# Kernel tuning notes

Measured on AMD Instinct MI355X. Metric: run time of the kernel, lower is better.

## Reference

```python
import jax, jax.numpy as jnp
import numpy as np

B, L, D = 4096, 200, 64
N_ITEMS, N_USERS, N_RATINGS = 100000, 100000, 5


def setup_inputs() -> dict:
    key = jax.random.key(0)
    ks = jax.random.split(key, 10)
    nodes = jax.random.randint(ks[0], (B,), 0, N_USERS)
    history_uv = jax.random.randint(ks[1], (B, L), 0, N_ITEMS)
    history_r = jax.random.randint(ks[2], (B, L), 0, N_RATINGS)
    s = 1.0 / np.sqrt(D)
    v2e = jax.random.normal(ks[3], (N_ITEMS, D), dtype=jnp.float32)
    r2e = jax.random.normal(ks[4], (N_RATINGS, D), dtype=jnp.float32)
    # torch Linear: weight is [out, in]
    w1_W = jax.random.uniform(ks[5], (D, 2 * D), dtype=jnp.float32, minval=-s, maxval=s)
    w1_b = jax.random.uniform(ks[6], (D,), dtype=jnp.float32, minval=-s, maxval=s)
    w2_W = jax.random.uniform(ks[7], (D, D), dtype=jnp.float32, minval=-s, maxval=s)
    w2_b = jax.random.uniform(ks[8], (D,), dtype=jnp.float32, minval=-s, maxval=s)
    return {
        "v2e": v2e, "r2e": r2e,
        "w1_W": w1_W, "w1_b": w1_b, "w2_W": w2_W, "w2_b": w2_b,
        "nodes": nodes, "history_uv": history_uv, "history_r": history_r,
    }


def reference(v2e, r2e, w1_W, w1_b, w2_W, w2_b, nodes, history_uv, history_r):
    # Gather item and rating embeddings for every (node, history slot): [B, L, D]
    e_uv = v2e[history_uv]
    e_r = r2e[history_r]
    # concat -> [B, L, 2D], two-layer MLP with ReLU
    x = jnp.concatenate([e_uv, e_r], axis=-1)
    h = jax.nn.relu(jnp.einsum("bli,oi->blo", x, w1_W) + w1_b)
    o = jax.nn.relu(jnp.einsum("bli,oi->blo", h, w2_W) + w2_b)
    # uv=True branch: plain mean over the history dimension (nodes/u2e unused)
    return jnp.mean(o, axis=1)  # [B, D]
```

## Files before the change

kernel.cpp:

```cpp
#include <hip/hip_runtime.h>

#define NITEMS 100000
#define NRATE  5
#define BB     4096
#define LL     200
#define DD     64
#define NTILES 6250
#define NWAVES 2048

typedef short short8  __attribute__((ext_vector_type(8)));
typedef float f32x4   __attribute__((ext_vector_type(4)));
typedef float f32x2   __attribute__((ext_vector_type(2)));
typedef int   i32x4   __attribute__((ext_vector_type(4)));
typedef int   i32x2   __attribute__((ext_vector_type(2)));

static __device__ __forceinline__ short f2bf(float f) {
  return (short)((__builtin_bit_cast(unsigned, f) + 0x8000u) >> 16);
}
static __device__ __forceinline__ unsigned pk2bf(float a, float b) {
  const unsigned ua = __builtin_bit_cast(unsigned, a) + 0x8000u;
  const unsigned ub = __builtin_bit_cast(unsigned, b) + 0x8000u;
  return __builtin_amdgcn_perm(ub, ua, 0x07060302u);
}
static __device__ __forceinline__ int kperm(int p) {
  return ((p & 3) << 4) | (p >> 2);
}

__global__ __launch_bounds__(256) void k_pre(
    const float* __restrict__ v2e, const float* __restrict__ r2e,
    const float* __restrict__ w1W, const float* __restrict__ w1b,
    const float* __restrict__ w2W,
    unsigned char* __restrict__ pre8, short* __restrict__ w2p,
    float* __restrict__ r5p)
{
  const int tid = threadIdx.x;
  const int blk = blockIdx.x;

  if (blk >= 512) {
    for (int idx = tid; idx < 64 * 64; idx += 256) {
      const int o = idx >> 6, p = idx & 63;
      w2p[idx] = f2bf(w2W[o * 64 + kperm(p)]);
    }
    for (int idx = tid; idx < NRATE * 64; idx += 256) {
      const int r = idx >> 6, p = idx & 63;
      const int o = kperm(p);
      const float4* wr = reinterpret_cast<const float4*>(w1W + o * 128 + 64);
      const float4* rr = reinterpret_cast<const float4*>(r2e + r * 64);
      float s = w1b[o];
#pragma unroll
      for (int q = 0; q < 16; ++q) {
        const float4 a = wr[q], b = rr[q];
        s += a.x * b.x + a.y * b.y + a.z * b.z + a.w * b.w;
      }
      r5p[r * 64 + p] = s;
    }
    return;
  }

  const int wave = tid >> 6, lane = tid & 63;
  const int n = lane & 15, quad = lane >> 4;
  const int gw = blk * 4 + wave;
  const int ntile = (gw < (NTILES - 3 * NWAVES)) ? 4 : 3;

  const int q0 = ((n >> 1) & 3) * 16 + (n >> 3) * 8 + (n & 1) * 4;

  short8 bfr[2][4];
#pragma unroll
  for (int nt = 0; nt < 4; ++nt)
#pragma unroll
    for (int kh = 0; kh < 2; ++kh) {
      const float4* p = reinterpret_cast<const float4*>(
          w1W + (nt * 16 + n) * 128 + kh * 32 + quad * 8);
      const float4 x0 = p[0], x1 = p[1];
      i32x4 pk = {(int)pk2bf(x0.x, x0.y), (int)pk2bf(x0.z, x0.w),
                  (int)pk2bf(x1.x, x1.y), (int)pk2bf(x1.z, x1.w)};
      bfr[kh][nt] = __builtin_bit_cast(short8, pk);
    }

  int tile = gw;
  float4 cur0, cur1, cur2, cur3;
  {
    const size_t row = (size_t)(tile * 16 + n);
    const float4* p = reinterpret_cast<const float4*>(v2e + row * 64 + quad * 8);
    cur0 = p[0]; cur1 = p[1];
    const float4* q = reinterpret_cast<const float4*>(v2e + row * 64 + 32 + quad * 8);
    cur2 = q[0]; cur3 = q[1];
  }

  for (int it = 0; it < ntile; ++it) {
    const int next = tile + NWAVES;
    float4 nx0, nx1, nx2, nx3;
    if (it + 1 < ntile) {
      const size_t row = (size_t)(next * 16 + n);
      const float4* p = reinterpret_cast<const float4*>(v2e + row * 64 + quad * 8);
      nx0 = p[0]; nx1 = p[1];
      const float4* q = reinterpret_cast<const float4*>(v2e + row * 64 + 32 + quad * 8);
      nx2 = q[0]; nx3 = q[1];
    }

    short8 afr[2];
    {
      i32x4 pk0 = {(int)pk2bf(cur0.x, cur0.y), (int)pk2bf(cur0.z, cur0.w),
                   (int)pk2bf(cur1.x, cur1.y), (int)pk2bf(cur1.z, cur1.w)};
      afr[0] = __builtin_bit_cast(short8, pk0);
      i32x4 pk1 = {(int)pk2bf(cur2.x, cur2.y), (int)pk2bf(cur2.z, cur2.w),
                   (int)pk2bf(cur3.x, cur3.y), (int)pk2bf(cur3.z, cur3.w)};
      afr[1] = __builtin_bit_cast(short8, pk1);
    }

    f32x4 d[4];
#pragma unroll
    for (int nt = 0; nt < 4; ++nt) {
      f32x4 z = {0.f, 0.f, 0.f, 0.f};
      z = __builtin_amdgcn_mfma_f32_16x16x32_bf16(afr[0], bfr[0][nt], z, 0, 0, 0);
      z = __builtin_amdgcn_mfma_f32_16x16x32_bf16(afr[1], bfr[1][nt], z, 0, 0, 0);
      d[nt] = z;
    }

    const int ib = tile * 16;
#pragma unroll
    for (int r = 0; r < 4; ++r) {
      const int item = ib + quad * 4 + r;
      int pkd = 0;
      pkd = __builtin_amdgcn_cvt_pk_fp8_f32(d[0][r], d[1][r], pkd, false);
      pkd = __builtin_amdgcn_cvt_pk_fp8_f32(d[2][r], d[3][r], pkd, true);
      *reinterpret_cast<int*>(pre8 + (size_t)item * 64 + q0) = pkd;
    }

    tile = next;
    cur0 = nx0; cur1 = nx1; cur2 = nx2; cur3 = nx3;
  }
}

__global__ __launch_bounds__(256) void k_main(
    const unsigned char* __restrict__ pre8, const float* __restrict__ r5p,
    const short* __restrict__ w2p, const float* __restrict__ w2b,
    const int* __restrict__ huv, const int* __restrict__ hrr,
    float* __restrict__ out)
{
  __shared__ __align__(16) float s_r5[4][5 * 68];

  const int tid  = threadIdx.x;
  const int wave = tid >> 6, lane = tid & 63;
  const int n = lane & 15, quad = lane >> 4;
  const int b = blockIdx.x * 4 + wave;

#pragma unroll
  for (int i = 0; i < 5; ++i) {
    const int idx = i * 64 + lane;
    s_r5[wave][(idx >> 6) * 68 + (idx & 63)] = r5p[idx];
  }

  const int* hu = huv + b * LL;
  const int* hr = hrr + b * LL;

  int iv[13], ir[13];
#pragma unroll
  for (int t = 0; t < 12; ++t) {
    iv[t] = hu[t * 16 + n];
    ir[t] = hr[t * 16 + n];
  }
  {
    const int lc = min(192 + n, LL - 1);
    iv[12] = hu[lc];
    ir[12] = hr[lc];
  }

  i32x4 g[13];
#pragma unroll
  for (int t = 0; t < 13; ++t)
    g[t] = *reinterpret_cast<const i32x4*>(
        pre8 + (size_t)iv[t] * 64 + quad * 16);

  short8 bfr[2][4];
#pragma unroll
  for (int nt = 0; nt < 4; ++nt)
#pragma unroll
    for (int kh = 0; kh < 2; ++kh)
      bfr[kh][nt] = *reinterpret_cast<const short8*>(
          w2p + (nt * 16 + n) * 64 + kh * 32 + quad * 8);

  f32x4 zb[4];
#pragma unroll
  for (int nt = 0; nt < 4; ++nt) {
    const float bv = w2b[nt * 16 + n];
    zb[nt] = f32x4{bv, bv, bv, bv};
  }

  const float tailm = (quad < 2) ? 1.0f : 0.0f;
  f32x2 acc2[4] = {{0.f, 0.f}, {0.f, 0.f}, {0.f, 0.f}, {0.f, 0.f}};

#pragma unroll
  for (int t = 0; t < 13; ++t) {
    const float* rbase = &s_r5[wave][ir[t] * 68 + quad * 8];
    short8 afr[2];
    {
      const f32x2* rp = reinterpret_cast<const f32x2*>(rbase);
      f32x2 p0 = __builtin_amdgcn_cvt_pk_f32_fp8(g[t][0], false) + rp[0];
      f32x2 p1 = __builtin_amdgcn_cvt_pk_f32_fp8(g[t][0], true)  + rp[1];
      f32x2 p2 = __builtin_amdgcn_cvt_pk_f32_fp8(g[t][1], false) + rp[2];
      f32x2 p3 = __builtin_amdgcn_cvt_pk_f32_fp8(g[t][1], true)  + rp[3];
      i32x4 hpk = {
        (int)pk2bf(fmaxf(p0.x, 0.f), fmaxf(p0.y, 0.f)),
        (int)pk2bf(fmaxf(p1.x, 0.f), fmaxf(p1.y, 0.f)),
        (int)pk2bf(fmaxf(p2.x, 0.f), fmaxf(p2.y, 0.f)),
        (int)pk2bf(fmaxf(p3.x, 0.f), fmaxf(p3.y, 0.f))};
      afr[0] = __builtin_bit_cast(short8, hpk);
    }
    {
      const f32x2* rp = reinterpret_cast<const f32x2*>(rbase + 32);
      f32x2 p0 = __builtin_amdgcn_cvt_pk_f32_fp8(g[t][2], false) + rp[0];
      f32x2 p1 = __builtin_amdgcn_cvt_pk_f32_fp8(g[t][2], true)  + rp[1];
      f32x2 p2 = __builtin_amdgcn_cvt_pk_f32_fp8(g[t][3], false) + rp[2];
      f32x2 p3 = __builtin_amdgcn_cvt_pk_f32_fp8(g[t][3], true)  + rp[3];
      i32x4 hpk = {
        (int)pk2bf(fmaxf(p0.x, 0.f), fmaxf(p0.y, 0.f)),
        (int)pk2bf(fmaxf(p1.x, 0.f), fmaxf(p1.y, 0.f)),
        (int)pk2bf(fmaxf(p2.x, 0.f), fmaxf(p2.y, 0.f)),
        (int)pk2bf(fmaxf(p3.x, 0.f), fmaxf(p3.y, 0.f))};
      afr[1] = __builtin_bit_cast(short8, hpk);
    }

    f32x4 d[4];
#pragma unroll
    for (int nt = 0; nt < 4; ++nt) {
      f32x4 z = zb[nt];
      z = __builtin_amdgcn_mfma_f32_16x16x32_bf16(afr[0], bfr[0][nt], z, 0, 0, 0);
      z = __builtin_amdgcn_mfma_f32_16x16x32_bf16(afr[1], bfr[1][nt], z, 0, 0, 0);
      d[nt] = z;
    }

#pragma unroll
    for (int nt = 0; nt < 4; ++nt) {
      const float m0 = fmaxf(d[nt][0], 0.f), m1 = fmaxf(d[nt][1], 0.f);
      const float m2 = fmaxf(d[nt][2], 0.f), m3 = fmaxf(d[nt][3], 0.f);
      f32x2 s = {m0 + m1, m2 + m3};
      if (t == 12) { s.x *= tailm; s.y *= tailm; }
      acc2[nt] += s;
    }
  }

  float acc[4];
#pragma unroll
  for (int nt = 0; nt < 4; ++nt) {
    float v = acc2[nt].x + acc2[nt].y;
    v += __shfl_xor(v, 16, 64);
    v += __shfl_xor(v, 32, 64);
    acc[nt] = v;
  }

  out[b * 64 + quad * 16 + n] = acc[quad] * (1.0f / (float)LL);
}

__global__ __launch_bounds__(256) void k_fallback(
    const float* __restrict__ v2e, const float* __restrict__ r2e,
    const float* __restrict__ w1W, const float* __restrict__ w1b,
    const float* __restrict__ w2W, const float* __restrict__ w2b,
    const int* __restrict__ huv, const int* __restrict__ hrr,
    float* __restrict__ out)
{
  __shared__ float sw1[64][129];
  __shared__ float sw2[64][65];
  __shared__ float sx[4][128];
  __shared__ float sh[4][64];
  __shared__ float red[4][64];

  const int tid = threadIdx.x;
  const int wave = tid >> 6, lane = tid & 63;
  const int b = blockIdx.x;

  for (int idx = tid; idx < 64 * 128; idx += 256) sw1[idx >> 7][idx & 127] = w1W[idx];
  for (int idx = tid; idx < 64 * 64; idx += 256) sw2[idx >> 6][idx & 63] = w2W[idx];
  __syncthreads();

  const float b1o = w1b[lane], b2o = w2b[lane];
  float acc = 0.f;

  for (int l = wave; l < LL; l += 4) {
    const int iv = huv[b * LL + l];
    const int ir = hrr[b * LL + l];
    sx[wave][lane]      = v2e[iv * 64 + lane];
    sx[wave][64 + lane] = r2e[ir * 64 + lane];
    __syncthreads();
    float h = b1o;
    for (int i = 0; i < 128; ++i) h += sx[wave][i] * sw1[lane][i];
    sh[wave][lane] = fmaxf(h, 0.f);
    __syncthreads();
    float o = b2o;
    for (int i = 0; i < 64; ++i) o += sh[wave][i] * sw2[lane][i];
    acc += fmaxf(o, 0.f);
  }

  red[wave][lane] = acc;
  __syncthreads();
  if (tid < 64) {
    const float s = red[0][tid] + red[1][tid] + red[2][tid] + red[3][tid];
    out[b * 64 + tid] = s * (1.0f / (float)LL);
  }
}

extern "C" void kernel_launch(void* const* d_in, const int* in_sizes, int n_in,
                              void* d_out, int out_size, void* d_ws, size_t ws_size,
                              hipStream_t stream) {
  (void)in_sizes; (void)n_in; (void)out_size;
  const float* v2e = (const float*)d_in[0];
  const float* r2e = (const float*)d_in[1];
  const float* w1W = (const float*)d_in[2];
  const float* w1b = (const float*)d_in[3];
  const float* w2W = (const float*)d_in[4];
  const float* w2b = (const float*)d_in[5];
  const int* huv = (const int*)d_in[7];
  const int* hrr = (const int*)d_in[8];
  float* out = (float*)d_out;

  const size_t OFF_R5 = (size_t)NITEMS * 64;
  const size_t OFF_W2 = OFF_R5 + NRATE * 64 * sizeof(float);
  const size_t NEED   = OFF_W2 + 64 * 64 * sizeof(short);

  if (ws_size >= NEED) {
    unsigned char* pre8 = (unsigned char*)d_ws;
    float* r5p = (float*)((char*)d_ws + OFF_R5);
    short* w2p = (short*)((char*)d_ws + OFF_W2);

    k_pre<<<513, 256, 0, stream>>>(v2e, r2e, w1W, w1b, w2W, pre8, w2p, r5p);
    k_main<<<BB / 4, 256, 0, stream>>>(pre8, r5p, w2p, w2b, huv, hrr, out);
  } else {
    k_fallback<<<BB, 256, 0, stream>>>(v2e, r2e, w1W, w1b, w2W, w2b, huv, hrr, out);
  }
}
```

Before: 114.0 us.

## Fuse precompute and main kernels into one cooperative launch with grid sync

Merges the item-table precompute kernel and the per-user aggregation kernel into one cooperative kernel of 768 persistent blocks separated by a grid-wide barrier. Block 0 builds the small rating and W2 tables while the other blocks split the 6250 item tiles. After the sync, each wave handles one or two batch rows. This removes a kernel launch and the gap between the two kernels, at the cost of a grid barrier and needing all 768 blocks resident (occupancy hint of 3 blocks per CU). It falls back to the two-kernel path if the cooperative launch fails.

Measured after the change: 199.2 us. 74.7% more time.

```diff
diff --git a/kernel.cpp b/kernel.cpp
--- a/kernel.cpp
+++ b/kernel.cpp
@@ -1,4 +1,7 @@
 #include <hip/hip_runtime.h>
+#include <hip/hip_cooperative_groups.h>
+
+namespace cg = cooperative_groups;
 
 #define NITEMS 100000
 #define NRATE  5
@@ -6,7 +9,10 @@
 #define LL     200
 #define DD     64
 #define NTILES 6250
-#define NWAVES 2048
+#define FB     768
+#define FWV    3068
+#define FXTRA  114
+#define P2W    3072
 
 typedef short short8  __attribute__((ext_vector_type(8)));
 typedef float f32x4   __attribute__((ext_vector_type(4)));
@@ -26,42 +32,36 @@
   return ((p & 3) << 4) | (p >> 2);
 }
 
-__global__ __launch_bounds__(256) void k_pre(
-    const float* __restrict__ v2e, const float* __restrict__ r2e,
-    const float* __restrict__ w1W, const float* __restrict__ w1b,
-    const float* __restrict__ w2W,
-    unsigned char* __restrict__ pre8, short* __restrict__ w2p,
-    float* __restrict__ r5p)
-{
-  const int tid = threadIdx.x;
-  const int blk = blockIdx.x;
-
-  if (blk >= 512) {
-    for (int idx = tid; idx < 64 * 64; idx += 256) {
-      const int o = idx >> 6, p = idx & 63;
-      w2p[idx] = f2bf(w2W[o * 64 + kperm(p)]);
-    }
-    for (int idx = tid; idx < NRATE * 64; idx += 256) {
-      const int r = idx >> 6, p = idx & 63;
-      const int o = kperm(p);
-      const float4* wr = reinterpret_cast<const float4*>(w1W + o * 128 + 64);
-      const float4* rr = reinterpret_cast<const float4*>(r2e + r * 64);
-      float s = w1b[o];
-#pragma unroll
-      for (int q = 0; q < 16; ++q) {
-        const float4 a = wr[q], b = rr[q];
-        s += a.x * b.x + a.y * b.y + a.z * b.z + a.w * b.w;
-      }
-      r5p[r * 64 + p] = s;
-    }
-    return;
-  }
-
-  const int wave = tid >> 6, lane = tid & 63;
-  const int n = lane & 15, quad = lane >> 4;
-  const int gw = blk * 4 + wave;
-  const int ntile = (gw < (NTILES - 3 * NWAVES)) ? 4 : 3;
-
+
+static __device__ __forceinline__ void do_small_tables(
+    int tid, const float* __restrict__ r2e, const float* __restrict__ w1W,
+    const float* __restrict__ w1b, const float* __restrict__ w2W,
+    short* __restrict__ w2p, float* __restrict__ r5p)
+{
+  for (int idx = tid; idx < 64 * 64; idx += 256) {
+    const int o = idx >> 6, p = idx & 63;
+    w2p[idx] = f2bf(w2W[o * 64 + kperm(p)]);
+  }
+  for (int idx = tid; idx < NRATE * 64; idx += 256) {
+    const int r = idx >> 6, p = idx & 63;
+    const int o = kperm(p);
+    const float4* wr = reinterpret_cast<const float4*>(w1W + o * 128 + 64);
+    const float4* rr = reinterpret_cast<const float4*>(r2e + r * 64);
+    float s = w1b[o];
+#pragma unroll
+    for (int q = 0; q < 16; ++q) {
+      const float4 a = wr[q], b = rr[q];
+      s += a.x * b.x + a.y * b.y + a.z * b.z + a.w * b.w;
+    }
+    r5p[r * 64 + p] = s;
+  }
+}
+
+static __device__ __forceinline__ void do_pre_tiles(
+    int n, int quad, const int* tiles, int ntc,
+    const float* __restrict__ v2e, const float* __restrict__ w1W,
+    unsigned char* __restrict__ pre8)
+{
   const int q0 = ((n >> 1) & 3) * 16 + (n >> 3) * 8 + (n & 1) * 4;
 
   short8 bfr[2][4];
@@ -77,21 +77,19 @@
       bfr[kh][nt] = __builtin_bit_cast(short8, pk);
     }
 
-  int tile = gw;
   float4 cur0, cur1, cur2, cur3;
   {
-    const size_t row = (size_t)(tile * 16 + n);
+    const size_t row = (size_t)(tiles[0] * 16 + n);
     const float4* p = reinterpret_cast<const float4*>(v2e + row * 64 + quad * 8);
     cur0 = p[0]; cur1 = p[1];
     const float4* q = reinterpret_cast<const float4*>(v2e + row * 64 + 32 + quad * 8);
     cur2 = q[0]; cur3 = q[1];
   }
 
-  for (int it = 0; it < ntile; ++it) {
-    const int next = tile + NWAVES;
+  for (int it = 0; it < ntc; ++it) {
     float4 nx0, nx1, nx2, nx3;
-    if (it + 1 < ntile) {
-      const size_t row = (size_t)(next * 16 + n);
+    if (it + 1 < ntc) {
+      const size_t row = (size_t)(tiles[it + 1] * 16 + n);
       const float4* p = reinterpret_cast<const float4*>(v2e + row * 64 + quad * 8);
       nx0 = p[0]; nx1 = p[1];
       const float4* q = reinterpret_cast<const float4*>(v2e + row * 64 + 32 + quad * 8);
@@ -117,7 +115,7 @@
       d[nt] = z;
     }
 
-    const int ib = tile * 16;
+    const int ib = tiles[it] * 16;
 #pragma unroll
     for (int r = 0; r < 4; ++r) {
       const int item = ib + quad * 4 + r;
@@ -127,30 +125,17 @@
       *reinterpret_cast<int*>(pre8 + (size_t)item * 64 + q0) = pkd;
     }
 
-    tile = next;
     cur0 = nx0; cur1 = nx1; cur2 = nx2; cur3 = nx3;
   }
 }
 
-__global__ __launch_bounds__(256) void k_main(
-    const unsigned char* __restrict__ pre8, const float* __restrict__ r5p,
-    const short* __restrict__ w2p, const float* __restrict__ w2b,
+static __device__ __forceinline__ void do_main_b(
+    int b, int n, int quad, const float* s_r5w,
+    const unsigned char* __restrict__ pre8,
+    const short8 bfr[2][4], const f32x4 zb[4], float tailm,
     const int* __restrict__ huv, const int* __restrict__ hrr,
     float* __restrict__ out)
 {
-  __shared__ __align__(16) float s_r5[4][5 * 68];
-
-  const int tid  = threadIdx.x;
-  const int wave = tid >> 6, lane = tid & 63;
-  const int n = lane & 15, quad = lane >> 4;
-  const int b = blockIdx.x * 4 + wave;
-
-#pragma unroll
-  for (int i = 0; i < 5; ++i) {
-    const int idx = i * 64 + lane;
-    s_r5[wave][(idx >> 6) * 68 + (idx & 63)] = r5p[idx];
-  }
-
   const int* hu = huv + b * LL;
   const int* hr = hrr + b * LL;
 
@@ -172,27 +157,11 @@
     g[t] = *reinterpret_cast<const i32x4*>(
         pre8 + (size_t)iv[t] * 64 + quad * 16);
 
-  short8 bfr[2][4];
-#pragma unroll
-  for (int nt = 0; nt < 4; ++nt)
-#pragma unroll
-    for (int kh = 0; kh < 2; ++kh)
-      bfr[kh][nt] = *reinterpret_cast<const short8*>(
-          w2p + (nt * 16 + n) * 64 + kh * 32 + quad * 8);
-
-  f32x4 zb[4];
-#pragma unroll
-  for (int nt = 0; nt < 4; ++nt) {
-    const float bv = w2b[nt * 16 + n];
-    zb[nt] = f32x4{bv, bv, bv, bv};
-  }
-
-  const float tailm = (quad < 2) ? 1.0f : 0.0f;
   f32x2 acc2[4] = {{0.f, 0.f}, {0.f, 0.f}, {0.f, 0.f}, {0.f, 0.f}};
 
 #pragma unroll
   for (int t = 0; t < 13; ++t) {
-    const float* rbase = &s_r5[wave][ir[t] * 68 + quad * 8];
+    const float* rbase = s_r5w + ir[t] * 68 + quad * 8;
     short8 afr[2];
     {
       const f32x2* rp = reinterpret_cast<const f32x2*>(rbase);
@@ -248,8 +217,116 @@
     v += __shfl_xor(v, 32, 64);
     acc[nt] = v;
   }
-
   out[b * 64 + quad * 16 + n] = acc[quad] * (1.0f / (float)LL);
+}
+
+__global__ __launch_bounds__(256, 3) void k_fused(
+    const float* __restrict__ v2e, const float* __restrict__ r2e,
+    const float* __restrict__ w1W, const float* __restrict__ w1b,
+    const float* __restrict__ w2W, const float* __restrict__ w2b,
+    const int* __restrict__ huv, const int* __restrict__ hrr,
+    unsigned char* __restrict__ pre8, short* __restrict__ w2p,
+    float* __restrict__ r5p, float* __restrict__ out)
+{
+  __shared__ __align__(16) float s_r5[4][5 * 68];
+
+  const int tid  = threadIdx.x;
+  const int blk  = blockIdx.x;
+  const int wave = tid >> 6, lane = tid & 63;
+  const int n = lane & 15, quad = lane >> 4;
+
+  if (blk == 0) {
+    do_small_tables(tid, r2e, w1W, w1b, w2W, w2p, r5p);
+  } else {
+    const int w = (blk - 1) * 4 + wave;
+    int tiles[3] = {w, w + FWV, w + 2 * FWV};
+    const int ntc = (w < FXTRA) ? 3 : 2;
+    do_pre_tiles(n, quad, tiles, ntc, v2e, w1W, pre8);
+  }
+
+  cg::this_grid().sync();
+
+#pragma unroll
+  for (int i = 0; i < 5; ++i) {
+    const int idx = i * 64 + lane;
+    s_r5[wave][(idx >> 6) * 68 + (idx & 63)] = r5p[idx];
+  }
+
+  short8 bfr[2][4];
+#pragma unroll
+  for (int nt = 0; nt < 4; ++nt)
+#pragma unroll
+    for (int kh = 0; kh < 2; ++kh)
+      bfr[kh][nt] = *reinterpret_cast<const short8*>(
+          w2p + (nt * 16 + n) * 64 + kh * 32 + quad * 8);
+
+  f32x4 zb[4];
+#pragma unroll
+  for (int nt = 0; nt < 4; ++nt) {
+    const float bv = w2b[nt * 16 + n];
+    zb[nt] = f32x4{bv, bv, bv, bv};
+  }
+  const float tailm = (quad < 2) ? 1.0f : 0.0f;
+
+  const int gw = blk * 4 + wave;
+  do_main_b(gw, n, quad, s_r5[wave], pre8, bfr, zb, tailm, huv, hrr, out);
+  if (gw < BB - P2W)
+    do_main_b(P2W + gw, n, quad, s_r5[wave], pre8, bfr, zb, tailm, huv, hrr, out);
+}
+
+__global__ __launch_bounds__(256) void k_pre(
+    const float* __restrict__ v2e, const float* __restrict__ r2e,
+    const float* __restrict__ w1W, const float* __restrict__ w1b,
+    const float* __restrict__ w2W,
+    unsigned char* __restrict__ pre8, short* __restrict__ w2p,
+    float* __restrict__ r5p)
+{
+  const int tid = threadIdx.x;
+  const int blk = blockIdx.x;
+  if (blk >= 512) {
+    do_small_tables(tid, r2e, w1W, w1b, w2W, w2p, r5p);
+    return;
+  }
+  const int wave = tid >> 6, lane = tid & 63;
+  const int n = lane & 15, quad = lane >> 4;
+  const int gw = blk * 4 + wave;
+  const int ntc = (gw < (NTILES - 3 * 2048)) ? 4 : 3;
+  int tiles[4] = {gw, gw + 2048, gw + 4096, gw + 6144};
+  do_pre_tiles(n, quad, tiles, ntc, v2e, w1W, pre8);
+}
+
+__global__ __launch_bounds__(256) void k_main(
+    const unsigned char* __restrict__ pre8, const float* __restrict__ r5p,
+    const short* __restrict__ w2p, const float* __restrict__ w2b,
+    const int* __restrict__ huv, const int* __restrict__ hrr,
+    float* __restrict__ out)
+{
+  __shared__ __align__(16) float s_r5[4][5 * 68];
+  const int tid  = threadIdx.x;
+  const int wave = tid >> 6, lane = tid & 63;
+  const int n = lane & 15, quad = lane >> 4;
+  const int b = blockIdx.x * 4 + wave;
+
+#pragma unroll
+  for (int i = 0; i < 5; ++i) {
+    const int idx = i * 64 + lane;
+    s_r5[wave][(idx >> 6) * 68 + (idx & 63)] = r5p[idx];
+  }
+  short8 bfr[2][4];
+#pragma unroll
+  for (int nt = 0; nt < 4; ++nt)
+#pragma unroll
+    for (int kh = 0; kh < 2; ++kh)
+      bfr[kh][nt] = *reinterpret_cast<const short8*>(
+          w2p + (nt * 16 + n) * 64 + kh * 32 + quad * 8);
+  f32x4 zb[4];
+#pragma unroll
+  for (int nt = 0; nt < 4; ++nt) {
+    const float bv = w2b[nt * 16 + n];
+    zb[nt] = f32x4{bv, bv, bv, bv};
+  }
+  const float tailm = (quad < 2) ? 1.0f : 0.0f;
+  do_main_b(b, n, quad, s_r5[wave], pre8, bfr, zb, tailm, huv, hrr, out);
 }
 
 __global__ __launch_bounds__(256) void k_fallback(
@@ -322,8 +399,15 @@
     float* r5p = (float*)((char*)d_ws + OFF_R5);
     short* w2p = (short*)((char*)d_ws + OFF_W2);
 
-    k_pre<<<513, 256, 0, stream>>>(v2e, r2e, w1W, w1b, w2W, pre8, w2p, r5p);
-    k_main<<<BB / 4, 256, 0, stream>>>(pre8, r5p, w2p, w2b, huv, hrr, out);
+    void* args[] = {(void*)&v2e, (void*)&r2e, (void*)&w1W, (void*)&w1b,
+                    (void*)&w2W, (void*)&w2b, (void*)&huv, (void*)&hrr,
+                    (void*)&pre8, (void*)&w2p, (void*)&r5p, (void*)&out};
+    hipError_t e = hipLaunchCooperativeKernel(
+        (const void*)k_fused, dim3(FB), dim3(256), args, 0, stream);
+    if (e != hipSuccess) {
+      k_pre<<<513, 256, 0, stream>>>(v2e, r2e, w1W, w1b, w2W, pre8, w2p, r5p);
+      k_main<<<BB / 4, 256, 0, stream>>>(pre8, r5p, w2p, w2b, huv, hrr, out);
+    }
   } else {
     k_fallback<<<BB, 256, 0, stream>>>(v2e, r2e, w1W, w1b, w2W, w2b, huv, hrr, out);
   }
```

## Gather fp8 rows with 4-byte coalesced loads staged through LDS, double-buffered

Applied to the files above, without the earlier changes.

Each gathered 64-byte fp8 row is now fetched by 16 lanes issuing 4-byte loads, with row indices broadcast by shuffle, instead of each lane issuing a 16-byte load from a scattered row. Rows pass through a per-wave LDS double buffer and are prefetched two steps ahead, replacing all 13 gathers being held in registers up front. The aim is better coalescing and lower register pressure, at the cost of LDS traffic, more load instructions and a shorter prefetch window. The pre-pass kernel is split into helper functions driven by a tile list, with the same behaviour.

Result: slower. 126.3 us (+10.7%).

```diff
diff --git a/kernel.cpp b/kernel.cpp
--- a/kernel.cpp
+++ b/kernel.cpp
@@ -6,7 +6,6 @@
 #define LL     200
 #define DD     64
 #define NTILES 6250
-#define NWAVES 2048
 
 typedef short short8  __attribute__((ext_vector_type(8)));
 typedef float f32x4   __attribute__((ext_vector_type(4)));
@@ -26,42 +25,36 @@
   return ((p & 3) << 4) | (p >> 2);
 }
 
-__global__ __launch_bounds__(256) void k_pre(
-    const float* __restrict__ v2e, const float* __restrict__ r2e,
-    const float* __restrict__ w1W, const float* __restrict__ w1b,
-    const float* __restrict__ w2W,
-    unsigned char* __restrict__ pre8, short* __restrict__ w2p,
-    float* __restrict__ r5p)
-{
-  const int tid = threadIdx.x;
-  const int blk = blockIdx.x;
-
-  if (blk >= 512) {
-    for (int idx = tid; idx < 64 * 64; idx += 256) {
-      const int o = idx >> 6, p = idx & 63;
-      w2p[idx] = f2bf(w2W[o * 64 + kperm(p)]);
-    }
-    for (int idx = tid; idx < NRATE * 64; idx += 256) {
-      const int r = idx >> 6, p = idx & 63;
-      const int o = kperm(p);
-      const float4* wr = reinterpret_cast<const float4*>(w1W + o * 128 + 64);
-      const float4* rr = reinterpret_cast<const float4*>(r2e + r * 64);
-      float s = w1b[o];
-#pragma unroll
-      for (int q = 0; q < 16; ++q) {
-        const float4 a = wr[q], b = rr[q];
-        s += a.x * b.x + a.y * b.y + a.z * b.z + a.w * b.w;
-      }
-      r5p[r * 64 + p] = s;
-    }
-    return;
-  }
-
-  const int wave = tid >> 6, lane = tid & 63;
-  const int n = lane & 15, quad = lane >> 4;
-  const int gw = blk * 4 + wave;
-  const int ntile = (gw < (NTILES - 3 * NWAVES)) ? 4 : 3;
-
+
+static __device__ __forceinline__ void do_small_tables(
+    int tid, const float* __restrict__ r2e, const float* __restrict__ w1W,
+    const float* __restrict__ w1b, const float* __restrict__ w2W,
+    short* __restrict__ w2p, float* __restrict__ r5p)
+{
+  for (int idx = tid; idx < 64 * 64; idx += 256) {
+    const int o = idx >> 6, p = idx & 63;
+    w2p[idx] = f2bf(w2W[o * 64 + kperm(p)]);
+  }
+  for (int idx = tid; idx < NRATE * 64; idx += 256) {
+    const int r = idx >> 6, p = idx & 63;
+    const int o = kperm(p);
+    const float4* wr = reinterpret_cast<const float4*>(w1W + o * 128 + 64);
+    const float4* rr = reinterpret_cast<const float4*>(r2e + r * 64);
+    float s = w1b[o];
+#pragma unroll
+    for (int q = 0; q < 16; ++q) {
+      const float4 a = wr[q], b = rr[q];
+      s += a.x * b.x + a.y * b.y + a.z * b.z + a.w * b.w;
+    }
+    r5p[r * 64 + p] = s;
+  }
+}
+
+static __device__ __forceinline__ void do_pre_tiles(
+    int n, int quad, const int* tiles, int ntc,
+    const float* __restrict__ v2e, const float* __restrict__ w1W,
+    unsigned char* __restrict__ pre8)
+{
   const int q0 = ((n >> 1) & 3) * 16 + (n >> 3) * 8 + (n & 1) * 4;
 
   short8 bfr[2][4];
@@ -77,21 +70,19 @@
       bfr[kh][nt] = __builtin_bit_cast(short8, pk);
     }
 
-  int tile = gw;
   float4 cur0, cur1, cur2, cur3;
   {
-    const size_t row = (size_t)(tile * 16 + n);
+    const size_t row = (size_t)(tiles[0] * 16 + n);
     const float4* p = reinterpret_cast<const float4*>(v2e + row * 64 + quad * 8);
     cur0 = p[0]; cur1 = p[1];
     const float4* q = reinterpret_cast<const float4*>(v2e + row * 64 + 32 + quad * 8);
     cur2 = q[0]; cur3 = q[1];
   }
 
-  for (int it = 0; it < ntile; ++it) {
-    const int next = tile + NWAVES;
+  for (int it = 0; it < ntc; ++it) {
     float4 nx0, nx1, nx2, nx3;
-    if (it + 1 < ntile) {
-      const size_t row = (size_t)(next * 16 + n);
+    if (it + 1 < ntc) {
+      const size_t row = (size_t)(tiles[it + 1] * 16 + n);
       const float4* p = reinterpret_cast<const float4*>(v2e + row * 64 + quad * 8);
       nx0 = p[0]; nx1 = p[1];
       const float4* q = reinterpret_cast<const float4*>(v2e + row * 64 + 32 + quad * 8);
@@ -117,7 +108,7 @@
       d[nt] = z;
     }
 
-    const int ib = tile * 16;
+    const int ib = tiles[it] * 16;
 #pragma unroll
     for (int r = 0; r < 4; ++r) {
       const int item = ib + quad * 4 + r;
@@ -127,9 +118,29 @@
       *reinterpret_cast<int*>(pre8 + (size_t)item * 64 + q0) = pkd;
     }
 
-    tile = next;
     cur0 = nx0; cur1 = nx1; cur2 = nx2; cur3 = nx3;
   }
+}
+
+__global__ __launch_bounds__(256) void k_pre(
+    const float* __restrict__ v2e, const float* __restrict__ r2e,
+    const float* __restrict__ w1W, const float* __restrict__ w1b,
+    const float* __restrict__ w2W,
+    unsigned char* __restrict__ pre8, short* __restrict__ w2p,
+    float* __restrict__ r5p)
+{
+  const int tid = threadIdx.x;
+  const int blk = blockIdx.x;
+  if (blk >= 512) {
+    do_small_tables(tid, r2e, w1W, w1b, w2W, w2p, r5p);
+    return;
+  }
+  const int wave = tid >> 6, lane = tid & 63;
+  const int n = lane & 15, quad = lane >> 4;
+  const int gw = blk * 4 + wave;
+  const int ntc = (gw < (NTILES - 3 * 2048)) ? 4 : 3;
+  int tiles[4] = {gw, gw + 2048, gw + 4096, gw + 6144};
+  do_pre_tiles(n, quad, tiles, ntc, v2e, w1W, pre8);
 }
 
 __global__ __launch_bounds__(256) void k_main(
@@ -139,6 +150,7 @@
     float* __restrict__ out)
 {
   __shared__ __align__(16) float s_r5[4][5 * 68];
+  __shared__ __align__(16) int   s_g[4][2][16 * 20];
 
   const int tid  = threadIdx.x;
   const int wave = tid >> 6, lane = tid & 63;
@@ -166,12 +178,6 @@
     ir[12] = hr[lc];
   }
 
-  i32x4 g[13];
-#pragma unroll
-  for (int t = 0; t < 13; ++t)
-    g[t] = *reinterpret_cast<const i32x4*>(
-        pre8 + (size_t)iv[t] * 64 + quad * 16);
-
   short8 bfr[2][4];
 #pragma unroll
   for (int nt = 0; nt < 4; ++nt)
@@ -186,20 +192,46 @@
     const float bv = w2b[nt * 16 + n];
     zb[nt] = f32x4{bv, bv, bv, bv};
   }
-
   const float tailm = (quad < 2) ? 1.0f : 0.0f;
+
+  int ga[2][4];
+#pragma unroll
+  for (int j = 0; j < 4; ++j) {
+    const int i0 = __shfl(iv[0], j * 4 + quad);
+    ga[0][j] = *reinterpret_cast<const int*>(pre8 + (size_t)i0 * 64 + n * 4);
+  }
+#pragma unroll
+  for (int j = 0; j < 4; ++j) {
+    const int i1 = __shfl(iv[1], j * 4 + quad);
+    ga[1][j] = *reinterpret_cast<const int*>(pre8 + (size_t)i1 * 64 + n * 4);
+  }
+
   f32x2 acc2[4] = {{0.f, 0.f}, {0.f, 0.f}, {0.f, 0.f}, {0.f, 0.f}};
 
 #pragma unroll
   for (int t = 0; t < 13; ++t) {
+    const int st = t & 1;
+    int* sg = s_g[wave][st];
+#pragma unroll
+    for (int j = 0; j < 4; ++j)
+      sg[(j * 4 + quad) * 20 + n] = ga[st][j];
+    if (t + 2 < 13) {
+#pragma unroll
+      for (int j = 0; j < 4; ++j) {
+        const int i2 = __shfl(iv[t + 2], j * 4 + quad);
+        ga[st][j] = *reinterpret_cast<const int*>(pre8 + (size_t)i2 * 64 + n * 4);
+      }
+    }
+    const i32x4 g = *reinterpret_cast<const i32x4*>(&sg[n * 20 + quad * 4]);
+
     const float* rbase = &s_r5[wave][ir[t] * 68 + quad * 8];
     short8 afr[2];
     {
       const f32x2* rp = reinterpret_cast<const f32x2*>(rbase);
-      f32x2 p0 = __builtin_amdgcn_cvt_pk_f32_fp8(g[t][0], false) + rp[0];
-      f32x2 p1 = __builtin_amdgcn_cvt_pk_f32_fp8(g[t][0], true)  + rp[1];
-      f32x2 p2 = __builtin_amdgcn_cvt_pk_f32_fp8(g[t][1], false) + rp[2];
-      f32x2 p3 = __builtin_amdgcn_cvt_pk_f32_fp8(g[t][1], true)  + rp[3];
+      f32x2 p0 = __builtin_amdgcn_cvt_pk_f32_fp8(g[0], false) + rp[0];
+      f32x2 p1 = __builtin_amdgcn_cvt_pk_f32_fp8(g[0], true)  + rp[1];
+      f32x2 p2 = __builtin_amdgcn_cvt_pk_f32_fp8(g[1], false) + rp[2];
+      f32x2 p3 = __builtin_amdgcn_cvt_pk_f32_fp8(g[1], true)  + rp[3];
       i32x4 hpk = {
         (int)pk2bf(fmaxf(p0.x, 0.f), fmaxf(p0.y, 0.f)),
         (int)pk2bf(fmaxf(p1.x, 0.f), fmaxf(p1.y, 0.f)),
@@ -209,10 +241,10 @@
     }
     {
       const f32x2* rp = reinterpret_cast<const f32x2*>(rbase + 32);
-      f32x2 p0 = __builtin_amdgcn_cvt_pk_f32_fp8(g[t][2], false) + rp[0];
-      f32x2 p1 = __builtin_amdgcn_cvt_pk_f32_fp8(g[t][2], true)  + rp[1];
-      f32x2 p2 = __builtin_amdgcn_cvt_pk_f32_fp8(g[t][3], false) + rp[2];
-      f32x2 p3 = __builtin_amdgcn_cvt_pk_f32_fp8(g[t][3], true)  + rp[3];
+      f32x2 p0 = __builtin_amdgcn_cvt_pk_f32_fp8(g[2], false) + rp[0];
+      f32x2 p1 = __builtin_amdgcn_cvt_pk_f32_fp8(g[2], true)  + rp[1];
+      f32x2 p2 = __builtin_amdgcn_cvt_pk_f32_fp8(g[3], false) + rp[2];
+      f32x2 p3 = __builtin_amdgcn_cvt_pk_f32_fp8(g[3], true)  + rp[3];
       i32x4 hpk = {
         (int)pk2bf(fmaxf(p0.x, 0.f), fmaxf(p0.y, 0.f)),
         (int)pk2bf(fmaxf(p1.x, 0.f), fmaxf(p1.y, 0.f)),
```
